# Performance work log

Hardware: AMD Instinct MI355X
Metric: run time of the kernel (lower is better)

## Reference

```python
import jax, jax.numpy as jnp
import numpy as np

B, H, W, NC = 8, 64, 64, 128
INTER = NC // 2
BN_EPS = 1e-4


def setup_inputs() -> dict:
    key = jax.random.key(0)
    ks = jax.random.split(key, 6)
    s_in = 1.0 / np.sqrt(NC)
    s_w = 1.0 / np.sqrt(INTER)
    return {
        "x": jax.random.normal(ks[0], (B, H, W, NC), jnp.float32),
        "theta_w": jax.random.normal(ks[1], (NC, INTER), jnp.float32) * s_in,
        "theta_b": jnp.zeros((INTER,), jnp.float32),
        "phi_w": jax.random.normal(ks[2], (NC, INTER), jnp.float32) * s_in,
        "phi_b": jnp.zeros((INTER,), jnp.float32),
        "g_w": jax.random.normal(ks[3], (NC, INTER), jnp.float32) * s_in,
        "g_b": jnp.zeros((INTER,), jnp.float32),
        "W_w": jax.random.normal(ks[4], (INTER, NC), jnp.float32) * s_w,
        "W_b": jnp.zeros((NC,), jnp.float32),
        "bn_gamma": jnp.ones((NC,), jnp.float32),
        "bn_beta": jnp.zeros((NC,), jnp.float32),
        "bn_mean": jnp.zeros((NC,), jnp.float32),
        "bn_var": jax.random.uniform(ks[5], (NC,), jnp.float32, 0.5, 1.5),
    }


def reference(x, theta_w, theta_b, phi_w, phi_b, g_w, g_b, W_w, W_b,
              bn_gamma, bn_beta, bn_mean, bn_var):
    b, h, w, c = x.shape
    n = h * w
    # 1x1 conv projections == per-pixel GEMMs; flatten spatial to tokens
    xt = x.reshape(b, n, c)                                  # [B, N, C]
    theta = xt @ theta_w + theta_b                           # [B, N, C']
    phi = xt @ phi_w + phi_b                                 # [B, N, C']
    g = xt @ g_w + g_b                                       # [B, N, C']
    # single-head, unscaled non-local attention
    f = jnp.einsum("bnc,bmc->bnm", theta, phi)               # [B, N, N]
    attn = jax.nn.softmax(f, axis=-1)
    y = jnp.einsum("bnm,bmc->bnc", attn, g)                  # [B, N, C']
    # W: 1x1 conv back to nc + BatchNorm (inference), then residual
    wy = y @ W_w + W_b                                       # [B, N, C]
    inv = bn_gamma * jax.lax.rsqrt(bn_var + BN_EPS)
    wy = (wy - bn_mean) * inv + bn_beta
    z = wy.reshape(b, h, w, c) + x
    return z
```

## Files before the change

### kernel.cpp

```cpp
#include <hip/hip_runtime.h>
#include <math.h>

typedef _Float16 v8h __attribute__((ext_vector_type(8)));
typedef __fp16 h2 __attribute__((ext_vector_type(2)));
typedef float v4f __attribute__((ext_vector_type(4)));
typedef float v16f __attribute__((ext_vector_type(16)));

#define MFMA32(a, b, c) __builtin_amdgcn_mfma_f32_32x32x16_f16((a), (b), (c), 0, 0, 0)
#define MFMA16(a, b, c) __builtin_amdgcn_mfma_f32_16x16x32_f16((a), (b), (c), 0, 0, 0)
#define ZV4 ((v4f){0.f, 0.f, 0.f, 0.f})
#define LOG2E 1.44269504f

#define TA64(row, colb)  ((((row) * 128) + (colb)) ^ (((row) & 7) << 4))
#define TA128(row, colb) ((((row) * 256) + (colb)) ^ (((row) & 15) << 4))

#define RAW_BARRIER() do {                                        \
    asm volatile("s_waitcnt lgkmcnt(0)" ::: "memory");            \
    asm volatile("s_barrier" ::: "memory");                       \
} while (0)

__device__ __forceinline__ unsigned int pk_f16(float a, float b) {
    return __builtin_bit_cast(unsigned int, __builtin_amdgcn_cvt_pkrtz(a, b));
}
__device__ __forceinline__ void pl32swap(unsigned int& a, unsigned int& b) {
    asm("v_permlane32_swap_b32 %0, %1" : "+v"(a), "+v"(b));
}
__device__ __forceinline__ float fexp2(float x) {
    float r;
    asm("v_exp_f32 %0, %1" : "=v"(r) : "v"(x));
    return r;
}

__global__ __launch_bounds__(256) void k_prep(
    const float* __restrict__ tw, const float* __restrict__ pw,
    const float* __restrict__ gw,
    const float* __restrict__ Ww, const float* __restrict__ Wb,
    const float* __restrict__ gamma, const float* __restrict__ beta,
    const float* __restrict__ mean, const float* __restrict__ var,
    _Float16* __restrict__ Wt, _Float16* __restrict__ wallT,
    float* __restrict__ sc, float* __restrict__ bi)
{
    int gid = blockIdx.x * 256 + threadIdx.x;
    #pragma unroll
    for (int r = 0; r < 2; ++r) {
        int idx = r * 4096 + gid;
        int d = idx >> 7, c = idx & 127;
        Wt[c * 64 + d] = (_Float16)Ww[idx];
    }
    #pragma unroll
    for (int r = 0; r < 6; ++r) {
        int idx = r * 4096 + gid;
        int p = idx >> 13, rem = idx & 8191;
        int o = rem >> 7, k = rem & 127;
        const float* wm = (p == 0) ? tw : (p == 1) ? pw : gw;
        wallT[idx] = (_Float16)wm[k * 64 + o];
    }
    if (blockIdx.x == 0 && threadIdx.x < 128) {
        int c = threadIdx.x;
        float inv = gamma[c] * rsqrtf(var[c] + 1e-4f);
        sc[c] = inv;
        bi[c] = (Wb[c] - mean[c]) * inv + beta[c];
    }
}

__global__ __launch_bounds__(512, 4) void k_proj(
    const float* __restrict__ x, const _Float16* __restrict__ wallT,
    const float* __restrict__ tb, const float* __restrict__ pb,
    const float* __restrict__ gb,
    _Float16* __restrict__ theta, _Float16* __restrict__ phi,
    _Float16* __restrict__ gT)
{
    __shared__ __align__(16) _Float16 tsc[8][16 * 72];
    __shared__ __align__(16) _Float16 gblk[64][136];
    const int t = threadIdx.x;
    const int w = t >> 6, l = t & 63, h = l >> 4, lo = l & 15;
    const int tok0 = blockIdx.x * 128 + w * 16;
    _Float16* tw_l = &tsc[w][0];

    v8h xA[4];
    #pragma unroll
    for (int kc = 0; kc < 4; ++kc) {
        const float* px = x + (size_t)(tok0 + lo) * 128 + kc * 32 + h * 8;
        float4 f0 = *(const float4*)(px);
        float4 f1 = *(const float4*)(px + 4);
        uint4 u;
        u.x = pk_f16(f0.x, f0.y); u.y = pk_f16(f0.z, f0.w);
        u.z = pk_f16(f1.x, f1.y); u.w = pk_f16(f1.z, f1.w);
        xA[kc] = __builtin_bit_cast(v8h, u);
    }

    #pragma unroll
    for (int p = 0; p < 2; ++p) {
        const _Float16* wp = wallT + p * 8192;
        const float* bias = (p == 0) ? tb : pb;
        _Float16* dst = (p == 0) ? theta : phi;
        const float scale = (p == 0) ? LOG2E : 1.0f;
        #pragma unroll
        for (int oc = 0; oc < 4; ++oc) {
            int o = oc * 16 + lo;
            v4f acc = ZV4;
            #pragma unroll
            for (int kc = 0; kc < 4; ++kc) {
                v8h B = *(const v8h*)(wp + o * 128 + kc * 32 + h * 8);
                acc = MFMA16(xA[kc], B, acc);
            }
            float bv = bias[o];
            #pragma unroll
            for (int rr = 0; rr < 4; ++rr)
                tw_l[(4 * h + rr) * 72 + o] = (_Float16)((acc[rr] + bv) * scale);
        }
        int token = l >> 2, c = l & 3;
        v8h v0 = *(const v8h*)&tw_l[token * 72 + c * 16];
        v8h v1 = *(const v8h*)&tw_l[token * 72 + c * 16 + 8];
        _Float16* dp = dst + (size_t)(tok0 + token) * 64 + c * 16;
        *(v8h*)(dp) = v0;
        *(v8h*)(dp + 8) = v1;
    }
    {
        const _Float16* wp = wallT + 2 * 8192;
        #pragma unroll
        for (int oc = 0; oc < 4; ++oc) {
            v4f acc = ZV4;
            #pragma unroll
            for (int kc = 0; kc < 4; ++kc) {
                v8h A = *(const v8h*)(wp + (oc * 16 + lo) * 128 + kc * 32 + h * 8);
                acc = MFMA16(A, xA[kc], acc);
            }
            #pragma unroll
            for (int rr = 0; rr < 4; ++rr) {
                int o = oc * 16 + 4 * h + rr;
                gblk[o][w * 16 + lo] = (_Float16)(acc[rr] + gb[o]);
            }
        }
    }
    __syncthreads();
    {
        int o = t >> 3, ch = t & 7;
        v8h v0 = *(const v8h*)&gblk[o][ch * 16];
        v8h v1 = *(const v8h*)&gblk[o][ch * 16 + 8];
        int tokg0 = blockIdx.x * 128;
        int bb = tokg0 >> 12, n0 = (tokg0 & 4095) + ch * 16;
        _Float16* gp = gT + ((size_t)bb * 64 + o) * 4096 + n0;
        *(v8h*)(gp) = v0;
        *(v8h*)(gp + 8) = v1;
    }
}

__global__ __launch_bounds__(512, 4) void k_attn(
    const _Float16* __restrict__ theta,
    const _Float16* __restrict__ phi,
    const _Float16* __restrict__ gT,
    const _Float16* __restrict__ Wt,
    const float* __restrict__ sc, const float* __restrict__ bi,
    const float* __restrict__ x, float* __restrict__ out)
{
    __shared__ __align__(16) _Float16 ldsbuf[32768];
    __shared__ float zf[8 * 32];

    const int t = threadIdx.x;
    const int w = t >> 6, l = t & 63, q32 = l & 31, hi2 = l >> 5;
    const int qt = w & 1, kh = w >> 1;
    const int bid = blockIdx.x;
    const int b = bid & 7, qb = bid >> 3;
    const size_t tok0 = (size_t)b * 4096 + qb * 64;
    const int tokA = (int)(qb * 64) + qt * 32;

    char* phB = (char*)ldsbuf;
    char* gvB = (char*)ldsbuf + 32768;

    v8h thB[4];
    #pragma unroll
    for (int kc = 0; kc < 4; ++kc)
        thB[kc] = *(const v8h*)(theta +
            (tok0 + qt * 32 + q32) * 64 + kc * 16 + hi2 * 8);

    const _Float16* phb = phi + (size_t)b * 4096 * 64;
    const _Float16* gvb = gT + (size_t)b * 64 * 4096;

    v16f yacc[2];
    #pragma unroll
    for (int df = 0; df < 2; ++df)
        #pragma unroll
        for (int r = 0; r < 16; ++r) yacc[df][r] = 0.f;
    float mrow = -INFINITY, lpart = 0.f;

    int qkRd[4], gvRd[2][2];
    #pragma unroll
    for (int kc = 0; kc < 4; ++kc)
        qkRd[kc] = TA64(kh * 32 + q32, (kc * 16 + hi2 * 8) * 2);
    #pragma unroll
    for (int df = 0; df < 2; ++df)
        #pragma unroll
        for (int s = 0; s < 2; ++s)
            gvRd[df][s] = TA128(df * 32 + q32, (kh * 32 + s * 16 + hi2 * 8) * 2);

    const int phA0 = TA64(t >> 3, (t & 7) * 16);
    const int phA1 = TA64((t >> 3) + 64, (t & 7) * 16);
    const int gvA0 = TA128(t >> 4, (t & 15) * 16);
    const int gvA1 = TA128((t >> 4) + 32, (t & 15) * 16);
    const _Float16* pPh = phb + (size_t)(t >> 3) * 64 + (t & 7) * 8;
    const _Float16* pGv = gvb + (size_t)(t >> 4) * 4096 + (t & 15) * 8;

    v8h pf0 = *(const v8h*)(pPh);
    v8h pf1 = *(const v8h*)(pPh + 64 * 64);
    v8h pf2 = *(const v8h*)(pGv);
    v8h pf3 = *(const v8h*)(pGv + (size_t)32 * 4096);
    pPh += 8192; pGv += 128;

    for (int kt = 0; kt < 32; ++kt) {
        char* phL = phB + (kt & 1) * 16384;
        char* gvL = gvB + (kt & 1) * 16384;
        *(v8h*)(phL + phA0) = pf0;
        *(v8h*)(phL + phA1) = pf1;
        *(v8h*)(gvL + gvA0) = pf2;
        *(v8h*)(gvL + gvA1) = pf3;
        if (kt < 31) {
            pf0 = *(const v8h*)(pPh);
            pf1 = *(const v8h*)(pPh + 64 * 64);
            pf2 = *(const v8h*)(pGv);
            pf3 = *(const v8h*)(pGv + (size_t)32 * 4096);
            pPh += 8192; pGv += 128;
        }
        RAW_BARRIER();
        v16f S;
        #pragma unroll
        for (int r = 0; r < 16; ++r) S[r] = 0.f;
        __builtin_amdgcn_s_setprio(1);
        #pragma unroll
        for (int kc = 0; kc < 4; ++kc) {
            v8h A = *(const v8h*)(phL + qkRd[kc]);
            S = MFMA32(A, thB[kc], S);
        }
        __builtin_amdgcn_s_setprio(0);
        float m0 = fmaxf(fmaxf(S[0], S[1]), S[2]);
        float m1 = fmaxf(fmaxf(S[3], S[4]), S[5]);
        float m2 = fmaxf(fmaxf(S[6], S[7]), S[8]);
        float m3 = fmaxf(fmaxf(S[9], S[10]), S[11]);
        float m4 = fmaxf(fmaxf(S[12], S[13]), S[14]);
        float vmax = fmaxf(fmaxf(fmaxf(m0, m1), fmaxf(m2, m3)),
                           fmaxf(m4, S[15]));
        vmax = fmaxf(vmax, __shfl_xor(vmax, 32));
        if (!__all(vmax <= mrow + 11.54f)) {
            float mn = fmaxf(mrow, vmax);
            float aa = fexp2(mrow - mn);
            mrow = mn;
            lpart *= aa;
            #pragma unroll
            for (int df = 0; df < 2; ++df)
                #pragma unroll
                for (int r = 0; r < 16; ++r)
                    yacc[df][r] *= aa;
        }
        float psum = 0.f;
        #pragma unroll
        for (int r = 0; r < 16; ++r) {
            S[r] = fexp2(S[r] - mrow);
            psum += S[r];
        }
        lpart += psum;
        unsigned int W0 = pk_f16(S[0], S[1]),   W1 = pk_f16(S[2], S[3]);
        unsigned int W2 = pk_f16(S[4], S[5]),   W3 = pk_f16(S[6], S[7]);
        unsigned int W4 = pk_f16(S[8], S[9]),   W5 = pk_f16(S[10], S[11]);
        unsigned int W6 = pk_f16(S[12], S[13]), W7 = pk_f16(S[14], S[15]);
        pl32swap(W0, W2); pl32swap(W1, W3);
        pl32swap(W4, W6); pl32swap(W5, W7);
        uint4 ub1; ub1.x = W0; ub1.y = W1; ub1.z = W2; ub1.w = W3;
        uint4 ub2; ub2.x = W4; ub2.y = W5; ub2.z = W6; ub2.w = W7;
        v8h pBv[2] = {__builtin_bit_cast(v8h, ub1), __builtin_bit_cast(v8h, ub2)};
        __builtin_amdgcn_s_setprio(1);
        #pragma unroll
        for (int df = 0; df < 2; ++df)
            #pragma unroll
            for (int s = 0; s < 2; ++s) {
                v8h A = *(const v8h*)(gvL + gvRd[df][s]);
                yacc[df] = MFMA32(A, pBv[s], yacc[df]);
            }
        __builtin_amdgcn_s_setprio(0);
    }

    __syncthreads();
    float lrow = lpart + __shfl_xor(lpart, 32);
    float inv = 1.0f / lrow;
    {
        char* slot = (char*)ldsbuf + w * 4096 + l * 64;
        #pragma unroll
        for (int j = 0; j < 4; ++j) {
            int df = j >> 1, r0 = (j & 1) * 8;
            uint4 u;
            u.x = pk_f16(yacc[df][r0 + 0] * inv, yacc[df][r0 + 1] * inv);
            u.y = pk_f16(yacc[df][r0 + 2] * inv, yacc[df][r0 + 3] * inv);
            u.z = pk_f16(yacc[df][r0 + 4] * inv, yacc[df][r0 + 5] * inv);
            u.w = pk_f16(yacc[df][r0 + 6] * inv, yacc[df][r0 + 7] * inv);
            *(uint4*)(slot + (j * 16 ^ ((l & 3) << 4))) = u;
        }
        zf[w * 32 + q32] = mrow + __log2f(lrow);
    }
    __syncthreads();
    if (w >= 2) return;

    float zq[4];
    #pragma unroll
    for (int kp = 0; kp < 4; ++kp) zq[kp] = zf[(kp * 2 + qt) * 32 + q32];
    float zmx = fmaxf(fmaxf(zq[0], zq[1]), fmaxf(zq[2], zq[3]));
    float wsum = 0.f;
    float yfin[2][16];
    #pragma unroll
    for (int df = 0; df < 2; ++df)
        #pragma unroll
        for (int r = 0; r < 16; ++r) yfin[df][r] = 0.f;
    #pragma unroll
    for (int kp = 0; kp < 4; ++kp) {
        char* slot = (char*)ldsbuf + (kp * 2 + qt) * 4096 + l * 64;
        float wk = fexp2(zq[kp] - zmx);
        wsum += wk;
        #pragma unroll
        for (int j = 0; j < 4; ++j) {
            v8h c = *(const v8h*)(slot + (j * 16 ^ ((l & 3) << 4)));
            int df = j >> 1, r0 = (j & 1) * 8;
            #pragma unroll
            for (int e = 0; e < 8; ++e)
                yfin[df][r0 + e] += wk * (float)c[e];
        }
    }
    float nrm = 1.0f / wsum;
    v8h yA[4];
    #pragma unroll
    for (int kc = 0; kc < 4; ++kc) {
        int df = kc >> 1, r0 = (kc & 1) * 8;
        unsigned int Wa = pk_f16(yfin[df][r0 + 0] * nrm, yfin[df][r0 + 1] * nrm);
        unsigned int Wb2 = pk_f16(yfin[df][r0 + 2] * nrm, yfin[df][r0 + 3] * nrm);
        unsigned int Wc = pk_f16(yfin[df][r0 + 4] * nrm, yfin[df][r0 + 5] * nrm);
        unsigned int Wd = pk_f16(yfin[df][r0 + 6] * nrm, yfin[df][r0 + 7] * nrm);
        pl32swap(Wa, Wc); pl32swap(Wb2, Wd);
        uint4 u; u.x = Wa; u.y = Wb2; u.z = Wc; u.w = Wd;
        yA[kc] = __builtin_bit_cast(v8h, u);
    }
    const float* xb = x + (size_t)b * 4096 * 128;
    float* ob = out + (size_t)b * 4096 * 128;
    #pragma unroll
    for (int cf = 0; cf < 4; ++cf) {
        int c = cf * 32 + q32;
        v16f wy;
        #pragma unroll
        for (int r = 0; r < 16; ++r) wy[r] = 0.f;
        #pragma unroll
        for (int kc = 0; kc < 4; ++kc) {
            v8h wB = *(const v8h*)(Wt + c * 64 + kc * 16 + hi2 * 8);
            wy = MFMA32(yA[kc], wB, wy);
        }
        float scc = sc[c], bic = bi[c];
        #pragma unroll
        for (int r = 0; r < 16; ++r) {
            int qrow = (r & 3) + 8 * (r >> 2) + 4 * hi2;
            size_t off = (size_t)(tokA + qrow) * 128 + c;
            ob[off] = wy[r] * scc + bic + xb[off];
        }
    }
}

extern "C" void kernel_launch(void* const* d_in, const int* in_sizes, int n_in,
                              void* d_out, int out_size, void* d_ws, size_t ws_size,
                              hipStream_t stream) {
    const float* x     = (const float*)d_in[0];
    const float* tw    = (const float*)d_in[1];
    const float* tb    = (const float*)d_in[2];
    const float* pw    = (const float*)d_in[3];
    const float* pb    = (const float*)d_in[4];
    const float* gw    = (const float*)d_in[5];
    const float* gb    = (const float*)d_in[6];
    const float* Ww    = (const float*)d_in[7];
    const float* Wb    = (const float*)d_in[8];
    const float* gamma = (const float*)d_in[9];
    const float* beta  = (const float*)d_in[10];
    const float* mean  = (const float*)d_in[11];
    const float* var   = (const float*)d_in[12];

    char* ws = (char*)d_ws;
    _Float16* theta = (_Float16*)ws;
    _Float16* phi   = (_Float16*)(ws + (4u << 20));
    _Float16* gT    = (_Float16*)(ws + (8u << 20));
    _Float16* Wt    = (_Float16*)(ws + (12u << 20));
    _Float16* wallT = (_Float16*)(ws + (12u << 20) + (1u << 16));
    float* sc       = (float*)(ws + (12u << 20) + (2u << 16));
    float* bi       = sc + 128;

    k_prep<<<16, 256, 0, stream>>>(tw, pw, gw, Ww, Wb, gamma, beta, mean, var,
                                   Wt, wallT, sc, bi);
    k_proj<<<256, 512, 0, stream>>>(x, wallT, tb, pb, gb, theta, phi, gT);
    k_attn<<<512, 512, 0, stream>>>(theta, phi, gT, Wt, sc, bi,
                                    x, (float*)d_out);
}
```

Measured before the change: 100.3 us.

## Process two query fragments per wave to reuse K/V tiles in attention

Each wave computes scores and PV accumulation for two 32-query fragments against the same phi/g LDS tiles, so a block covers 128 queries and the grid halves. This halves phi/g global loads and LDS reads per query. The cost is twice the accumulator registers, lower occupancy (launch bounds 2), and fewer blocks than before, which may leave CUs underused.

```diff
diff --git a/kernel.cpp b/kernel.cpp
--- a/kernel.cpp
+++ b/kernel.cpp
@@ -146,7 +146,7 @@
     }
 }
 
-__global__ __launch_bounds__(512, 4) void k_attn(
+__global__ __launch_bounds__(512, 2) void k_attn(
     const _Float16* __restrict__ theta,
     const _Float16* __restrict__ phi,
     const _Float16* __restrict__ gT,
@@ -155,34 +155,37 @@
     const float* __restrict__ x, float* __restrict__ out)
 {
     __shared__ __align__(16) _Float16 ldsbuf[32768];
-    __shared__ float zf[8 * 32];
+    __shared__ float zf[8 * 64];
 
     const int t = threadIdx.x;
     const int w = t >> 6, l = t & 63, q32 = l & 31, hi2 = l >> 5;
-    const int qt = w & 1, kh = w >> 1;
+    const int qp = w & 1, kh = w >> 1;
     const int bid = blockIdx.x;
     const int b = bid & 7, qb = bid >> 3;
-    const size_t tok0 = (size_t)b * 4096 + qb * 64;
-    const int tokA = (int)(qb * 64) + qt * 32;
+    const size_t tok0 = (size_t)b * 4096 + qb * 128;
 
     char* phB = (char*)ldsbuf;
     char* gvB = (char*)ldsbuf + 32768;
 
-    v8h thB[4];
-    #pragma unroll
-    for (int kc = 0; kc < 4; ++kc)
-        thB[kc] = *(const v8h*)(theta +
-            (tok0 + qt * 32 + q32) * 64 + kc * 16 + hi2 * 8);
+    v8h thB[2][4];
+    #pragma unroll
+    for (int f = 0; f < 2; ++f)
+        #pragma unroll
+        for (int kc = 0; kc < 4; ++kc)
+            thB[f][kc] = *(const v8h*)(theta +
+                (tok0 + qp * 64 + f * 32 + q32) * 64 + kc * 16 + hi2 * 8);
 
     const _Float16* phb = phi + (size_t)b * 4096 * 64;
     const _Float16* gvb = gT + (size_t)b * 64 * 4096;
 
-    v16f yacc[2];
-    #pragma unroll
-    for (int df = 0; df < 2; ++df)
-        #pragma unroll
-        for (int r = 0; r < 16; ++r) yacc[df][r] = 0.f;
-    float mrow = -INFINITY, lpart = 0.f;
+    v16f yacc[2][2];
+    #pragma unroll
+    for (int f = 0; f < 2; ++f)
+        #pragma unroll
+        for (int df = 0; df < 2; ++df)
+            #pragma unroll
+            for (int r = 0; r < 16; ++r) yacc[f][df][r] = 0.f;
+    float mrow[2] = {-INFINITY, -INFINITY}, lpart[2] = {0.f, 0.f};
 
     int qkRd[4], gvRd[2][2];
     #pragma unroll
@@ -222,138 +225,169 @@
             pPh += 8192; pGv += 128;
         }
         RAW_BARRIER();
-        v16f S;
-        #pragma unroll
-        for (int r = 0; r < 16; ++r) S[r] = 0.f;
+        v16f S0, S1;
+        #pragma unroll
+        for (int r = 0; r < 16; ++r) { S0[r] = 0.f; S1[r] = 0.f; }
         __builtin_amdgcn_s_setprio(1);
         #pragma unroll
         for (int kc = 0; kc < 4; ++kc) {
             v8h A = *(const v8h*)(phL + qkRd[kc]);
-            S = MFMA32(A, thB[kc], S);
+            S0 = MFMA32(A, thB[0][kc], S0);
+            S1 = MFMA32(A, thB[1][kc], S1);
         }
         __builtin_amdgcn_s_setprio(0);
-        float m0 = fmaxf(fmaxf(S[0], S[1]), S[2]);
-        float m1 = fmaxf(fmaxf(S[3], S[4]), S[5]);
-        float m2 = fmaxf(fmaxf(S[6], S[7]), S[8]);
-        float m3 = fmaxf(fmaxf(S[9], S[10]), S[11]);
-        float m4 = fmaxf(fmaxf(S[12], S[13]), S[14]);
-        float vmax = fmaxf(fmaxf(fmaxf(m0, m1), fmaxf(m2, m3)),
-                           fmaxf(m4, S[15]));
-        vmax = fmaxf(vmax, __shfl_xor(vmax, 32));
-        if (!__all(vmax <= mrow + 11.54f)) {
-            float mn = fmaxf(mrow, vmax);
-            float aa = fexp2(mrow - mn);
-            mrow = mn;
-            lpart *= aa;
-            #pragma unroll
-            for (int df = 0; df < 2; ++df)
+        float vmax[2];
+        {
+            float a0 = fmaxf(fmaxf(S0[0], S0[1]), S0[2]);
+            float a1 = fmaxf(fmaxf(S0[3], S0[4]), S0[5]);
+            float a2 = fmaxf(fmaxf(S0[6], S0[7]), S0[8]);
+            float a3 = fmaxf(fmaxf(S0[9], S0[10]), S0[11]);
+            float a4 = fmaxf(fmaxf(S0[12], S0[13]), S0[14]);
+            float v = fmaxf(fmaxf(fmaxf(a0, a1), fmaxf(a2, a3)),
+                            fmaxf(a4, S0[15]));
+            vmax[0] = fmaxf(v, __shfl_xor(v, 32));
+        }
+        {
+            float a0 = fmaxf(fmaxf(S1[0], S1[1]), S1[2]);
+            float a1 = fmaxf(fmaxf(S1[3], S1[4]), S1[5]);
+            float a2 = fmaxf(fmaxf(S1[6], S1[7]), S1[8]);
+            float a3 = fmaxf(fmaxf(S1[9], S1[10]), S1[11]);
+            float a4 = fmaxf(fmaxf(S1[12], S1[13]), S1[14]);
+            float v = fmaxf(fmaxf(fmaxf(a0, a1), fmaxf(a2, a3)),
+                            fmaxf(a4, S1[15]));
+            vmax[1] = fmaxf(v, __shfl_xor(v, 32));
+        }
+        bool ok = (vmax[0] <= mrow[0] + 11.54f) && (vmax[1] <= mrow[1] + 11.54f);
+        if (!__all(ok)) {
+            #pragma unroll
+            for (int f = 0; f < 2; ++f) {
+                float mn = fmaxf(mrow[f], vmax[f]);
+                float aa = fexp2(mrow[f] - mn);
+                mrow[f] = mn;
+                lpart[f] *= aa;
                 #pragma unroll
-                for (int r = 0; r < 16; ++r)
-                    yacc[df][r] *= aa;
-        }
-        float psum = 0.f;
-        #pragma unroll
-        for (int r = 0; r < 16; ++r) {
-            S[r] = fexp2(S[r] - mrow);
-            psum += S[r];
-        }
-        lpart += psum;
-        unsigned int W0 = pk_f16(S[0], S[1]),   W1 = pk_f16(S[2], S[3]);
-        unsigned int W2 = pk_f16(S[4], S[5]),   W3 = pk_f16(S[6], S[7]);
-        unsigned int W4 = pk_f16(S[8], S[9]),   W5 = pk_f16(S[10], S[11]);
-        unsigned int W6 = pk_f16(S[12], S[13]), W7 = pk_f16(S[14], S[15]);
-        pl32swap(W0, W2); pl32swap(W1, W3);
-        pl32swap(W4, W6); pl32swap(W5, W7);
-        uint4 ub1; ub1.x = W0; ub1.y = W1; ub1.z = W2; ub1.w = W3;
-        uint4 ub2; ub2.x = W4; ub2.y = W5; ub2.z = W6; ub2.w = W7;
-        v8h pBv[2] = {__builtin_bit_cast(v8h, ub1), __builtin_bit_cast(v8h, ub2)};
+                for (int df = 0; df < 2; ++df)
+                    #pragma unroll
+                    for (int r = 0; r < 16; ++r)
+                        yacc[f][df][r] *= aa;
+            }
+        }
+        v8h pB[2][2];
+        #pragma unroll
+        for (int f = 0; f < 2; ++f) {
+            v16f& S = (f == 0) ? S0 : S1;
+            float psum = 0.f;
+            #pragma unroll
+            for (int r = 0; r < 16; ++r) {
+                S[r] = fexp2(S[r] - mrow[f]);
+                psum += S[r];
+            }
+            lpart[f] += psum;
+            unsigned int W0 = pk_f16(S[0], S[1]),   W1 = pk_f16(S[2], S[3]);
+            unsigned int W2 = pk_f16(S[4], S[5]),   W3 = pk_f16(S[6], S[7]);
+            unsigned int W4 = pk_f16(S[8], S[9]),   W5 = pk_f16(S[10], S[11]);
+            unsigned int W6 = pk_f16(S[12], S[13]), W7 = pk_f16(S[14], S[15]);
+            pl32swap(W0, W2); pl32swap(W1, W3);
+            pl32swap(W4, W6); pl32swap(W5, W7);
+            uint4 u1; u1.x = W0; u1.y = W1; u1.z = W2; u1.w = W3;
+            uint4 u2; u2.x = W4; u2.y = W5; u2.z = W6; u2.w = W7;
+            pB[f][0] = __builtin_bit_cast(v8h, u1);
+            pB[f][1] = __builtin_bit_cast(v8h, u2);
+        }
         __builtin_amdgcn_s_setprio(1);
         #pragma unroll
         for (int df = 0; df < 2; ++df)
             #pragma unroll
             for (int s = 0; s < 2; ++s) {
                 v8h A = *(const v8h*)(gvL + gvRd[df][s]);
-                yacc[df] = MFMA32(A, pBv[s], yacc[df]);
+                yacc[0][df] = MFMA32(A, pB[0][s], yacc[0][df]);
+                yacc[1][df] = MFMA32(A, pB[1][s], yacc[1][df]);
             }
         __builtin_amdgcn_s_setprio(0);
     }
 
     __syncthreads();
-    float lrow = lpart + __shfl_xor(lpart, 32);
-    float inv = 1.0f / lrow;
-    {
-        char* slot = (char*)ldsbuf + w * 4096 + l * 64;
+    #pragma unroll
+    for (int f = 0; f < 2; ++f) {
+        float lrow = lpart[f] + __shfl_xor(lpart[f], 32);
+        float inv = 1.0f / lrow;
+        char* slot = (char*)ldsbuf + w * 8192 + f * 4096 + l * 64;
         #pragma unroll
         for (int j = 0; j < 4; ++j) {
             int df = j >> 1, r0 = (j & 1) * 8;
             uint4 u;
-            u.x = pk_f16(yacc[df][r0 + 0] * inv, yacc[df][r0 + 1] * inv);
-            u.y = pk_f16(yacc[df][r0 + 2] * inv, yacc[df][r0 + 3] * inv);
-            u.z = pk_f16(yacc[df][r0 + 4] * inv, yacc[df][r0 + 5] * inv);
-            u.w = pk_f16(yacc[df][r0 + 6] * inv, yacc[df][r0 + 7] * inv);
+            u.x = pk_f16(yacc[f][df][r0 + 0] * inv, yacc[f][df][r0 + 1] * inv);
+            u.y = pk_f16(yacc[f][df][r0 + 2] * inv, yacc[f][df][r0 + 3] * inv);
+            u.z = pk_f16(yacc[f][df][r0 + 4] * inv, yacc[f][df][r0 + 5] * inv);
+            u.w = pk_f16(yacc[f][df][r0 + 6] * inv, yacc[f][df][r0 + 7] * inv);
             *(uint4*)(slot + (j * 16 ^ ((l & 3) << 4))) = u;
         }
-        zf[w * 32 + q32] = mrow + __log2f(lrow);
+        zf[(w * 2 + f) * 32 + q32] = mrow[f] + __log2f(lrow);
     }
     __syncthreads();
     if (w >= 2) return;
 
-    float zq[4];
-    #pragma unroll
-    for (int kp = 0; kp < 4; ++kp) zq[kp] = zf[(kp * 2 + qt) * 32 + q32];
-    float zmx = fmaxf(fmaxf(zq[0], zq[1]), fmaxf(zq[2], zq[3]));
-    float wsum = 0.f;
-    float yfin[2][16];
-    #pragma unroll
-    for (int df = 0; df < 2; ++df)
-        #pragma unroll
-        for (int r = 0; r < 16; ++r) yfin[df][r] = 0.f;
-    #pragma unroll
-    for (int kp = 0; kp < 4; ++kp) {
-        char* slot = (char*)ldsbuf + (kp * 2 + qt) * 4096 + l * 64;
-        float wk = fexp2(zq[kp] - zmx);
-        wsum += wk;
-        #pragma unroll
-        for (int j = 0; j < 4; ++j) {
-            v8h c = *(const v8h*)(slot + (j * 16 ^ ((l & 3) << 4)));
-            int df = j >> 1, r0 = (j & 1) * 8;
-            #pragma unroll
-            for (int e = 0; e < 8; ++e)
-                yfin[df][r0 + e] += wk * (float)c[e];
-        }
-    }
-    float nrm = 1.0f / wsum;
-    v8h yA[4];
-    #pragma unroll
-    for (int kc = 0; kc < 4; ++kc) {
-        int df = kc >> 1, r0 = (kc & 1) * 8;
-        unsigned int Wa = pk_f16(yfin[df][r0 + 0] * nrm, yfin[df][r0 + 1] * nrm);
-        unsigned int Wb2 = pk_f16(yfin[df][r0 + 2] * nrm, yfin[df][r0 + 3] * nrm);
-        unsigned int Wc = pk_f16(yfin[df][r0 + 4] * nrm, yfin[df][r0 + 5] * nrm);
-        unsigned int Wd = pk_f16(yfin[df][r0 + 6] * nrm, yfin[df][r0 + 7] * nrm);
-        pl32swap(Wa, Wc); pl32swap(Wb2, Wd);
-        uint4 u; u.x = Wa; u.y = Wb2; u.z = Wc; u.w = Wd;
-        yA[kc] = __builtin_bit_cast(v8h, u);
-    }
-    const float* xb = x + (size_t)b * 4096 * 128;
-    float* ob = out + (size_t)b * 4096 * 128;
-    #pragma unroll
-    for (int cf = 0; cf < 4; ++cf) {
-        int c = cf * 32 + q32;
-        v16f wy;
-        #pragma unroll
-        for (int r = 0; r < 16; ++r) wy[r] = 0.f;
+    #pragma unroll
+    for (int f = 0; f < 2; ++f) {
+        float zq[4];
+        #pragma unroll
+        for (int kp = 0; kp < 4; ++kp)
+            zq[kp] = zf[((kp * 2 + w) * 2 + f) * 32 + q32];
+        float zmx = fmaxf(fmaxf(zq[0], zq[1]), fmaxf(zq[2], zq[3]));
+        float wsum = 0.f;
+        float yfin[2][16];
+        #pragma unroll
+        for (int df = 0; df < 2; ++df)
+            #pragma unroll
+            for (int r = 0; r < 16; ++r) yfin[df][r] = 0.f;
+        #pragma unroll
+        for (int kp = 0; kp < 4; ++kp) {
+            char* slot = (char*)ldsbuf + (kp * 2 + w) * 8192 + f * 4096 + l * 64;
+            float wk = fexp2(zq[kp] - zmx);
+            wsum += wk;
+            #pragma unroll
+            for (int j = 0; j < 4; ++j) {
+                v8h c = *(const v8h*)(slot + (j * 16 ^ ((l & 3) << 4)));
+                int df = j >> 1, r0 = (j & 1) * 8;
+                #pragma unroll
+                for (int e = 0; e < 8; ++e)
+                    yfin[df][r0 + e] += wk * (float)c[e];
+            }
+        }
+        float nrm = 1.0f / wsum;
+        v8h yA[4];
         #pragma unroll
         for (int kc = 0; kc < 4; ++kc) {
-            v8h wB = *(const v8h*)(Wt + c * 64 + kc * 16 + hi2 * 8);
-            wy = MFMA32(yA[kc], wB, wy);
-        }
-        float scc = sc[c], bic = bi[c];
-        #pragma unroll
-        for (int r = 0; r < 16; ++r) {
-            int qrow = (r & 3) + 8 * (r >> 2) + 4 * hi2;
-            size_t off = (size_t)(tokA + qrow) * 128 + c;
-            ob[off] = wy[r] * scc + bic + xb[off];
+            int df = kc >> 1, r0 = (kc & 1) * 8;
+            unsigned int Wa = pk_f16(yfin[df][r0 + 0] * nrm, yfin[df][r0 + 1] * nrm);
+            unsigned int Wb2 = pk_f16(yfin[df][r0 + 2] * nrm, yfin[df][r0 + 3] * nrm);
+            unsigned int Wc = pk_f16(yfin[df][r0 + 4] * nrm, yfin[df][r0 + 5] * nrm);
+            unsigned int Wd = pk_f16(yfin[df][r0 + 6] * nrm, yfin[df][r0 + 7] * nrm);
+            pl32swap(Wa, Wc); pl32swap(Wb2, Wd);
+            uint4 u; u.x = Wa; u.y = Wb2; u.z = Wc; u.w = Wd;
+            yA[kc] = __builtin_bit_cast(v8h, u);
+        }
+        const int tokA = qb * 128 + w * 64 + f * 32;
+        const float* xb = x + (size_t)b * 4096 * 128;
+        float* ob = out + (size_t)b * 4096 * 128;
+        #pragma unroll
+        for (int cf = 0; cf < 4; ++cf) {
+            int c = cf * 32 + q32;
+            v16f wy;
+            #pragma unroll
+            for (int r = 0; r < 16; ++r) wy[r] = 0.f;
+            #pragma unroll
+            for (int kc = 0; kc < 4; ++kc) {
+                v8h wB = *(const v8h*)(Wt + c * 64 + kc * 16 + hi2 * 8);
+                wy = MFMA32(yA[kc], wB, wy);
+            }
+            float scc = sc[c], bic = bi[c];
+            #pragma unroll
+            for (int r = 0; r < 16; ++r) {
+                int qrow = (r & 3) + 8 * (r >> 2) + 4 * hi2;
+                size_t off = (size_t)(tokA + qrow) * 128 + c;
+                ob[off] = wy[r] * scc + bic + xb[off];
+            }
         }
     }
 }
@@ -387,6 +421,6 @@
     k_prep<<<16, 256, 0, stream>>>(tw, pw, gw, Ww, Wb, gamma, beta, mean, var,
                                    Wt, wallT, sc, bi);
     k_proj<<<256, 512, 0, stream>>>(x, wallT, tb, pb, gb, theta, phi, gT);
-    k_attn<<<512, 512, 0, stream>>>(theta, phi, gT, Wt, sc, bi,
+    k_attn<<<256, 512, 0, stream>>>(theta, phi, gT, Wt, sc, bi,
                                     x, (float*)d_out);
 }
```

Measured after the change: 82.72 us. 1.21x faster.
